# Optimization experiments

Hardware: AMD Instinct MI355X
Metric: run time of the kernel (lower is better)

The kernel has to match this reference:

```python
import jax, jax.numpy as jnp
import numpy as np

B, H, S, D = 4, 16, 2048, 64


def setup_inputs() -> dict:
    key = jax.random.key(0)
    kq, kk, kv, kp = jax.random.split(key, 4)
    query = jax.random.normal(kq, (B, H, S, D), dtype=jnp.float32)
    k = jax.random.normal(kk, (B, H, S, D), dtype=jnp.float32)
    value = jax.random.normal(kv, (B, H, S, D), dtype=jnp.float32)
    # 0/1 key-padding mask, broadcastable against the [S, S] causal mask
    padding_mask = jax.random.randint(kp, (B, 1, 1, S), 0, 2, dtype=jnp.int32)
    return {"query": query, "key": k, "value": value, "padding_mask": padding_mask}


def reference(query, key, value, padding_mask):
    d_k = query.shape[-1]
    seq_len = query.shape[-2]
    # scores: [B, H, S, S]
    scores = jnp.einsum("bhqd,bhkd->bhqk", query, key) / jnp.sqrt(jnp.float32(d_k))
    # causal mask: 1 above diagonal
    future = jnp.triu(jnp.ones((seq_len, seq_len), dtype=jnp.float32), k=1)
    combined = future + padding_mask.astype(jnp.float32)  # values in {0,1,2}
    # faithful to torch masked_fill(combined_mask == 1, -1e9): only exact 1 is masked
    scores = jnp.where(combined == 1.0, jnp.float32(-1e9), scores)
    attention_weights = jax.nn.softmax(scores, axis=-1)
    result = attention_weights @ value  # [B, H, S, D]
    return result, attention_weights
```

## Files before the change

### kernel.cpp

```cpp
#include <hip/hip_runtime.h>

#define SEQ 2048
#define DH  64
#define NH  16
#define NB  4
#define QT  64
#define NT  512
#define NHEADS (NB * NH)
#define NKT (SEQ / 64)
#define NBLK (NHEADS * (SEQ / QT))
#define TILE_ELEMS 4096

typedef _Float16 f16x8 __attribute__((ext_vector_type(8)));
typedef short    s16x8 __attribute__((ext_vector_type(8)));
typedef float    f32x4 __attribute__((ext_vector_type(4)));

static __device__ __forceinline__ int swe(int row, int col) {
    return (row << 6) + (col ^ ((row & 7) << 3));
}

static __device__ __forceinline__ void gload16(const void* g, void* l) {
    __builtin_amdgcn_global_load_lds(
        (const __attribute__((address_space(1))) void*)g,
        (__attribute__((address_space(3))) void*)l, 16, 0, 0);
}

static __device__ __forceinline__ short f16b(float x) {
    _Float16 h = (_Float16)x;
    return __builtin_bit_cast(short, h);
}

__global__ __launch_bounds__(256) void prep(
    const float* __restrict__ K, const float* __restrict__ V,
    const int* __restrict__ pad,
    short* __restrict__ kh, short* __restrict__ kl,
    short* __restrict__ vh, short* __restrict__ vl,
    unsigned* __restrict__ pm)
{
    const int t    = threadIdx.x;
    const int kt   = blockIdx.x & (NKT - 1);
    const int head = blockIdx.x >> 5;
    const size_t toff = ((size_t)head * NKT + kt) * TILE_ELEMS;
    const float* Kg = K + ((size_t)head * SEQ + (size_t)kt * 64) * DH;
    const float* Vg = V + ((size_t)head * SEQ + (size_t)kt * 64) * DH;

    {
        const int row = t >> 2;
        const int c0  = (t & 3) * 16;
        const float4* gp = (const float4*)(Kg + (size_t)row * DH + c0);
        const float4 v0 = gp[0], v1 = gp[1], v2 = gp[2], v3 = gp[3];
        const float x[16] = {v0.x,v0.y,v0.z,v0.w, v1.x,v1.y,v1.z,v1.w,
                             v2.x,v2.y,v2.z,v2.w, v3.x,v3.y,v3.z,v3.w};
        s16x8 hi[2], lo[2];
#pragma unroll
        for (int j = 0; j < 16; ++j) {
            _Float16 h = (_Float16)x[j];
            hi[j >> 3][j & 7] = __builtin_bit_cast(short, h);
            lo[j >> 3][j & 7] = f16b(x[j] - (float)h);
        }
        *(s16x8*)&kh[toff + swe(row, c0)]     = hi[0];
        *(s16x8*)&kh[toff + swe(row, c0 + 8)] = hi[1];
        *(s16x8*)&kl[toff + swe(row, c0)]     = lo[0];
        *(s16x8*)&kl[toff + swe(row, c0 + 8)] = lo[1];
    }
    {
#pragma unroll
        for (int half = 0; half < 2; ++half) {
            const int d  = t & 63;
            const int k0 = half * 32 + (t >> 6) * 8;
            s16x8 hi8, lo8;
#pragma unroll
            for (int i = 0; i < 8; ++i) {
                float x = Vg[(size_t)(k0 + i) * DH + d];
                _Float16 h = (_Float16)x;
                hi8[i] = __builtin_bit_cast(short, h);
                lo8[i] = f16b(x - (float)h);
            }
            *(s16x8*)&vh[toff + swe(d, k0)] = hi8;
            *(s16x8*)&vl[toff + swe(d, k0)] = lo8;
        }
    }
    if (blockIdx.x == 0) {
        const int b = t >> 6, klc = t & 63;
        unsigned mword = 0;
#pragma unroll
        for (int kt2 = 0; kt2 < NKT; ++kt2)
            mword |= (unsigned)(pad[b * SEQ + kt2 * 64 + klc] & 1) << kt2;
        pm[t] = mword;
    }
}

#define QK_TILE(kb_, A0, A1) do {                                                    \
  _Pragma("unroll") for (int dh = 0; dh < 2; ++dh) {                                 \
    const int d0_ = dh * 32 + lg * 8;                                                \
    const f16x8 bh = *(const f16x8*)&s_k[kb_][0][swe(key, d0_)];                     \
    const f16x8 bl = *(const f16x8*)&s_k[kb_][1][swe(key, d0_)];                     \
    A0 = __builtin_amdgcn_mfma_f32_16x16x32_f16(qfh[0][dh], bh, A0, 0, 0, 0);        \
    A1 = __builtin_amdgcn_mfma_f32_16x16x32_f16(qfh[1][dh], bh, A1, 0, 0, 0);        \
    A0 = __builtin_amdgcn_mfma_f32_16x16x32_f16(qfh[0][dh], bl, A0, 0, 0, 0);        \
    A1 = __builtin_amdgcn_mfma_f32_16x16x32_f16(qfh[1][dh], bl, A1, 0, 0, 0);        \
    A0 = __builtin_amdgcn_mfma_f32_16x16x32_f16(qfl[0][dh], bh, A0, 0, 0, 0);        \
    A1 = __builtin_amdgcn_mfma_f32_16x16x32_f16(qfl[1][dh], bh, A1, 0, 0, 0);        \
  } } while (0)

#define STAGE_K(buf_, kt_) do {                                                      \
    const size_t o_ = (size_t)(kt_) * TILE_ELEMS + (size_t)t * 8;                    \
    gload16(khh + o_, &s_k[buf_][0][w * 512]);                                       \
    gload16(klh + o_, &s_k[buf_][1][w * 512]);                                       \
} while (0)
#define STAGE_V(buf_, kt_) do {                                                      \
    const size_t o_ = (size_t)(kt_) * TILE_ELEMS + (size_t)t * 8;                    \
    gload16(vhh + o_, &s_vu.v[buf_][0][w * 512]);                                    \
    gload16(vlh + o_, &s_vu.v[buf_][1][w * 512]);                                    \
} while (0)

#define WAIT_BAR(cnt_) do {                                                          \
    asm volatile("s_waitcnt " cnt_ ::: "memory");                                    \
    __builtin_amdgcn_s_barrier();                                                    \
    __builtin_amdgcn_sched_barrier(0);                                               \
} while (0)

__global__ __launch_bounds__(NT, 4) void attn_fwd(
    const float* __restrict__ Q,
    const short* __restrict__ KH, const short* __restrict__ KL,
    const short* __restrict__ VH, const short* __restrict__ VL,
    const unsigned* __restrict__ PM,
    float* __restrict__ out_res, float* __restrict__ out_w)
{
    __shared__ __attribute__((aligned(16))) short s_k[2][2][TILE_ELEMS];
    __shared__ union __attribute__((aligned(16))) {
        short v[2][2][TILE_ELEMS];
        short q[2][TILE_ELEMS];
        float o[64][68];
    } s_vu;
    __shared__ __attribute__((aligned(16))) short s_w[TILE_ELEMS];
    __shared__ float s_red[64][4];

    const int t = threadIdx.x;
    int bid = blockIdx.x;
    bid = (bid & 7) * (NBLK / 8) + (bid >> 3);

    const int qtile = bid & (SEQ / QT - 1);
    const int head  = bid >> 5;
    const int q0    = qtile * QT;
    const size_t hoff = (size_t)head * SEQ * DH;
    const size_t woff = (size_t)head * SEQ * SEQ;

    const short* khh = KH + (size_t)head * NKT * TILE_ELEMS;
    const short* klh = KL + (size_t)head * NKT * TILE_ELEMS;
    const short* vhh = VH + (size_t)head * NKT * TILE_ELEMS;
    const short* vlh = VL + (size_t)head * NKT * TILE_ELEMS;

    const int l  = t & 63;
    const int w  = t >> 6;
    const int wq = w >> 2;
    const int wk = w & 3;
    const int lj = l & 15;
    const int lg = l >> 4;

    const int key = wk * 16 + lj;
    const unsigned pmask = PM[(head >> 4) * 64 + key];

    {
        const int row = t >> 3;
        const int c0  = (t & 7) * 8;
        const float* gp = Q + hoff + (size_t)(q0 + row) * DH + c0;
        const float4 a = *(const float4*)gp;
        const float4 b = *(const float4*)(gp + 4);
        const float x[8] = {a.x,a.y,a.z,a.w, b.x,b.y,b.z,b.w};
        s16x8 hi8, lo8;
#pragma unroll
        for (int j = 0; j < 8; ++j) {
            _Float16 h = (_Float16)x[j];
            hi8[j] = __builtin_bit_cast(short, h);
            lo8[j] = f16b(x[j] - (float)h);
        }
        *(s16x8*)&s_vu.q[0][swe(row, c0)] = hi8;
        *(s16x8*)&s_vu.q[1][swe(row, c0)] = lo8;
    }
    __syncthreads();

    f16x8 qfh[2][2], qfl[2][2];
#pragma unroll
    for (int m = 0; m < 2; ++m)
#pragma unroll
        for (int dh = 0; dh < 2; ++dh) {
            const int row = wq * 32 + m * 16 + lj;
            const int d0  = dh * 32 + lg * 8;
            qfh[m][dh] = *(const f16x8*)&s_vu.q[0][swe(row, d0)];
            qfl[m][dh] = *(const f16x8*)&s_vu.q[1][swe(row, d0)];
        }
    asm volatile("s_waitcnt lgkmcnt(0)" ::: "memory");
    __syncthreads();

    const int wk2   = wk >> 1;
    const int dbase = (wk & 1) * 32;
    const int ks    = wk2 * 32 + lg * 8;

    float rs[2][4] = {};
    f32x4 ov[2][2];
#pragma unroll
    for (int m = 0; m < 2; ++m)
#pragma unroll
        for (int n = 0; n < 2; ++n) ov[m][n] = (f32x4){0.f,0.f,0.f,0.f};

    STAGE_K(0, 0);
    STAGE_V(0, 0);
    WAIT_BAR("vmcnt(0)");

#pragma unroll 1
    for (int kt = 0; kt < NKT; ++kt) {
        const int cur = kt & 1, nxt = cur ^ 1;
        const int ktn = (kt + 1) & (NKT - 1);
        STAGE_K(nxt, ktn);
        STAGE_V(nxt, ktn);

        f32x4 a0 = {0.f,0.f,0.f,0.f}, a1 = {0.f,0.f,0.f,0.f};
        __builtin_amdgcn_s_setprio(1);
        QK_TILE(cur, a0, a1);
        __builtin_amdgcn_s_setprio(0);

        const int ka = kt * 64 + key;
        const int pd = (int)((pmask >> kt) & 1u);
#pragma unroll
        for (int m = 0; m < 2; ++m) {
            const f32x4 av = m ? a1 : a0;
            const int qrow = q0 + wq * 32 + m * 16 + lg * 4;
            const int qloc = wq * 32 + m * 16 + lg * 4;
#pragma unroll
            for (int r = 0; r < 4; ++r) {
                const bool msk = ((ka > qrow + r) != (pd == 1));
                const float s  = msk ? -8.0e9f : av[r];
                const float e  = __expf(s * 0.125f);
                rs[m][r] += e;
                s_w[swe(qloc + r, key)] = f16b(e);
            }
        }
        WAIT_BAR("lgkmcnt(0)");

        {
            const f16x8 aw0 = *(const f16x8*)&s_w[swe(wq * 32 + lj,      ks)];
            const f16x8 aw1 = *(const f16x8*)&s_w[swe(wq * 32 + 16 + lj, ks)];
            const f16x8 bh0 = *(const f16x8*)&s_vu.v[cur][0][swe(dbase + lj,      ks)];
            const f16x8 bh1 = *(const f16x8*)&s_vu.v[cur][0][swe(dbase + 16 + lj, ks)];
            const f16x8 bl0 = *(const f16x8*)&s_vu.v[cur][1][swe(dbase + lj,      ks)];
            const f16x8 bl1 = *(const f16x8*)&s_vu.v[cur][1][swe(dbase + 16 + lj, ks)];
            __builtin_amdgcn_s_setprio(1);
            ov[0][0] = __builtin_amdgcn_mfma_f32_16x16x32_f16(aw0, bh0, ov[0][0], 0,0,0);
            ov[0][1] = __builtin_amdgcn_mfma_f32_16x16x32_f16(aw0, bh1, ov[0][1], 0,0,0);
            ov[1][0] = __builtin_amdgcn_mfma_f32_16x16x32_f16(aw1, bh0, ov[1][0], 0,0,0);
            ov[1][1] = __builtin_amdgcn_mfma_f32_16x16x32_f16(aw1, bh1, ov[1][1], 0,0,0);
            ov[0][0] = __builtin_amdgcn_mfma_f32_16x16x32_f16(aw0, bl0, ov[0][0], 0,0,0);
            ov[0][1] = __builtin_amdgcn_mfma_f32_16x16x32_f16(aw0, bl1, ov[0][1], 0,0,0);
            ov[1][0] = __builtin_amdgcn_mfma_f32_16x16x32_f16(aw1, bl0, ov[1][0], 0,0,0);
            ov[1][1] = __builtin_amdgcn_mfma_f32_16x16x32_f16(aw1, bl1, ov[1][1], 0,0,0);
            __builtin_amdgcn_s_setprio(0);
        }
        WAIT_BAR("vmcnt(0)");
    }

#pragma unroll
    for (int m = 0; m < 2; ++m)
#pragma unroll
        for (int r = 0; r < 4; ++r) {
            float v = rs[m][r];
#pragma unroll
            for (int off = 1; off < 16; off <<= 1) v += __shfl_xor(v, off, 64);
            rs[m][r] = v;
        }
    if (lj == 0) {
#pragma unroll
        for (int m = 0; m < 2; ++m)
#pragma unroll
            for (int r = 0; r < 4; ++r)
                s_red[wq * 32 + m * 16 + lg * 4 + r][wk] = rs[m][r];
    }
    __syncthreads();
    float invr[2][4];
#pragma unroll
    for (int m = 0; m < 2; ++m)
#pragma unroll
        for (int r = 0; r < 4; ++r) {
            const int row = wq * 32 + m * 16 + lg * 4 + r;
            invr[m][r] = 1.0f / (s_red[row][0] + s_red[row][1] +
                                 s_red[row][2] + s_red[row][3]);
        }

#pragma unroll
    for (int m = 0; m < 2; ++m)
#pragma unroll
        for (int n = 0; n < 2; ++n)
#pragma unroll
            for (int r = 0; r < 4; ++r) ov[m][n][r] *= invr[m][r];

    if (wk2 == 0) {
#pragma unroll
        for (int m = 0; m < 2; ++m)
#pragma unroll
            for (int n = 0; n < 2; ++n)
#pragma unroll
                for (int r = 0; r < 4; ++r)
                    s_vu.o[wq * 32 + m * 16 + lg * 4 + r][dbase + n * 16 + lj] = ov[m][n][r];
    }
    __syncthreads();
    if (wk2 == 1) {
#pragma unroll
        for (int m = 0; m < 2; ++m)
#pragma unroll
            for (int n = 0; n < 2; ++n)
#pragma unroll
                for (int r = 0; r < 4; ++r)
                    s_vu.o[wq * 32 + m * 16 + lg * 4 + r][dbase + n * 16 + lj] += ov[m][n][r];
    }
    __syncthreads();
    {
        const int row = t >> 3;
        const int c0  = (t & 7) * 8;
        const float4 v0 = *(const float4*)&s_vu.o[row][c0];
        const float4 v1 = *(const float4*)&s_vu.o[row][c0 + 4];
        float* op = out_res + hoff + (size_t)(q0 + row) * DH + c0;
        *(float4*)op       = v0;
        *(float4*)(op + 4) = v1;
    }

#pragma unroll 1
    for (int kt = 0; kt < NKT; ++kt) {
        const int cur = kt & 1, nxt = cur ^ 1;
        STAGE_K(nxt, (kt + 1) & (NKT - 1));

        f32x4 a0 = {0.f,0.f,0.f,0.f}, a1 = {0.f,0.f,0.f,0.f};
        __builtin_amdgcn_s_setprio(1);
        QK_TILE(cur, a0, a1);
        __builtin_amdgcn_s_setprio(0);

        const int ka = kt * 64 + key;
        const int pd = (int)((pmask >> kt) & 1u);
#pragma unroll
        for (int m = 0; m < 2; ++m) {
            const f32x4 av = m ? a1 : a0;
            const int qrow = q0 + wq * 32 + m * 16 + lg * 4;
#pragma unroll
            for (int r = 0; r < 4; ++r) {
                const bool msk = ((ka > qrow + r) != (pd == 1));
                const float s  = msk ? -8.0e9f : av[r];
                const float e  = __expf(s * 0.125f);
                out_w[woff + (size_t)(qrow + r) * SEQ + ka] = e * invr[m][r];
            }
        }
        WAIT_BAR("vmcnt(8)");
    }
}

extern "C" void kernel_launch(void* const* d_in, const int* in_sizes, int n_in,
                              void* d_out, int out_size, void* d_ws, size_t ws_size,
                              hipStream_t stream) {
    const float* Q   = (const float*)d_in[0];
    const float* K   = (const float*)d_in[1];
    const float* V   = (const float*)d_in[2];
    const int*   pad = (const int*)d_in[3];
    float* out_res = (float*)d_out;
    float* out_w   = out_res + (size_t)NB * NH * SEQ * DH;

    const size_t T = (size_t)NHEADS * NKT * TILE_ELEMS;
    short* kh = (short*)d_ws;
    short* kl = kh + T;
    short* vh = kl + T;
    short* vl = vh + T;
    unsigned* pm = (unsigned*)(vl + T);

    prep<<<dim3(NHEADS * NKT), 256, 0, stream>>>(K, V, pad, kh, kl, vh, vl, pm);
    attn_fwd<<<dim3(NBLK), NT, 0, stream>>>(Q, kh, kl, vh, vl, pm, out_res, out_w);
}
```

Baseline: 1.466 ms.

## Software-pipeline PV matmul one tile behind QK and use nontemporal weight stores

The first pass now double-buffers the softmax weight tile and runs the P·V MFMAs for the previous key tile after computing QK for the current one, so each iteration needs one barrier instead of two. V loads are issued per tile just after the barrier, and the first K load is moved ahead of the Q conversion. The second pass moves its barrier to the top of the loop, and the attention-weight writes become nontemporal stores to avoid polluting cache. Shared memory is reorganised: s_red now aliases the weight buffer and the output staging aliases the V buffers. V now has less lead time before it is consumed, which could expose load latency.

New measurement: 1.376 ms. 1.06x faster.

```diff
diff --git a/kernel.cpp b/kernel.cpp
--- a/kernel.cpp
+++ b/kernel.cpp
@@ -103,6 +103,25 @@
     A1 = __builtin_amdgcn_mfma_f32_16x16x32_f16(qfl[1][dh], bh, A1, 0, 0, 0);        \
   } } while (0)
 
+#define PV_TILE(prv_) do {                                                           \
+    const f16x8 aw0 = *(const f16x8*)&s_wq.w[prv_][swe(wq * 32 + lj,      ks)];      \
+    const f16x8 aw1 = *(const f16x8*)&s_wq.w[prv_][swe(wq * 32 + 16 + lj, ks)];      \
+    const f16x8 bh0 = *(const f16x8*)&s_vo.v[prv_][0][swe(dbase + lj,      ks)];     \
+    const f16x8 bh1 = *(const f16x8*)&s_vo.v[prv_][0][swe(dbase + 16 + lj, ks)];     \
+    const f16x8 bl0 = *(const f16x8*)&s_vo.v[prv_][1][swe(dbase + lj,      ks)];     \
+    const f16x8 bl1 = *(const f16x8*)&s_vo.v[prv_][1][swe(dbase + 16 + lj, ks)];     \
+    __builtin_amdgcn_s_setprio(1);                                                   \
+    ov[0][0] = __builtin_amdgcn_mfma_f32_16x16x32_f16(aw0, bh0, ov[0][0], 0,0,0);    \
+    ov[0][1] = __builtin_amdgcn_mfma_f32_16x16x32_f16(aw0, bh1, ov[0][1], 0,0,0);    \
+    ov[1][0] = __builtin_amdgcn_mfma_f32_16x16x32_f16(aw1, bh0, ov[1][0], 0,0,0);    \
+    ov[1][1] = __builtin_amdgcn_mfma_f32_16x16x32_f16(aw1, bh1, ov[1][1], 0,0,0);    \
+    ov[0][0] = __builtin_amdgcn_mfma_f32_16x16x32_f16(aw0, bl0, ov[0][0], 0,0,0);    \
+    ov[0][1] = __builtin_amdgcn_mfma_f32_16x16x32_f16(aw0, bl1, ov[0][1], 0,0,0);    \
+    ov[1][0] = __builtin_amdgcn_mfma_f32_16x16x32_f16(aw1, bl0, ov[1][0], 0,0,0);    \
+    ov[1][1] = __builtin_amdgcn_mfma_f32_16x16x32_f16(aw1, bl1, ov[1][1], 0,0,0);    \
+    __builtin_amdgcn_s_setprio(0);                                                   \
+} while (0)
+
 #define STAGE_K(buf_, kt_) do {                                                      \
     const size_t o_ = (size_t)(kt_) * TILE_ELEMS + (size_t)t * 8;                    \
     gload16(khh + o_, &s_k[buf_][0][w * 512]);                                       \
@@ -110,11 +129,11 @@
 } while (0)
 #define STAGE_V(buf_, kt_) do {                                                      \
     const size_t o_ = (size_t)(kt_) * TILE_ELEMS + (size_t)t * 8;                    \
-    gload16(vhh + o_, &s_vu.v[buf_][0][w * 512]);                                    \
-    gload16(vlh + o_, &s_vu.v[buf_][1][w * 512]);                                    \
+    gload16(vhh + o_, &s_vo.v[buf_][0][w * 512]);                                    \
+    gload16(vlh + o_, &s_vo.v[buf_][1][w * 512]);                                    \
 } while (0)
 
-#define WAIT_BAR(cnt_) do {                                                          \
+#define PIPE_BAR(cnt_) do {                                                          \
     asm volatile("s_waitcnt " cnt_ ::: "memory");                                    \
     __builtin_amdgcn_s_barrier();                                                    \
     __builtin_amdgcn_sched_barrier(0);                                               \
@@ -130,11 +149,13 @@
     __shared__ __attribute__((aligned(16))) short s_k[2][2][TILE_ELEMS];
     __shared__ union __attribute__((aligned(16))) {
         short v[2][2][TILE_ELEMS];
+        float o[64][68];
+    } s_vo;
+    __shared__ union __attribute__((aligned(16))) {
+        short w[2][TILE_ELEMS];
         short q[2][TILE_ELEMS];
-        float o[64][68];
-    } s_vu;
-    __shared__ __attribute__((aligned(16))) short s_w[TILE_ELEMS];
-    __shared__ float s_red[64][4];
+    } s_wq;
+    float (*s_red)[4] = reinterpret_cast<float (*)[4]>(&s_wq.w[0][0]);
 
     const int t = threadIdx.x;
     int bid = blockIdx.x;
@@ -160,6 +181,12 @@
 
     const int key = wk * 16 + lj;
     const unsigned pmask = PM[(head >> 4) * 64 + key];
+
+    const int wk2   = wk >> 1;
+    const int dbase = (wk & 1) * 32;
+    const int ks    = wk2 * 32 + lg * 8;
+
+    STAGE_K(0, 0);
 
     {
         const int row = t >> 3;
@@ -175,8 +202,8 @@
             hi8[j] = __builtin_bit_cast(short, h);
             lo8[j] = f16b(x[j] - (float)h);
         }
-        *(s16x8*)&s_vu.q[0][swe(row, c0)] = hi8;
-        *(s16x8*)&s_vu.q[1][swe(row, c0)] = lo8;
+        *(s16x8*)&s_wq.q[0][swe(row, c0)] = hi8;
+        *(s16x8*)&s_wq.q[1][swe(row, c0)] = lo8;
     }
     __syncthreads();
 
@@ -187,15 +214,11 @@
         for (int dh = 0; dh < 2; ++dh) {
             const int row = wq * 32 + m * 16 + lj;
             const int d0  = dh * 32 + lg * 8;
-            qfh[m][dh] = *(const f16x8*)&s_vu.q[0][swe(row, d0)];
-            qfl[m][dh] = *(const f16x8*)&s_vu.q[1][swe(row, d0)];
+            qfh[m][dh] = *(const f16x8*)&s_wq.q[0][swe(row, d0)];
+            qfl[m][dh] = *(const f16x8*)&s_wq.q[1][swe(row, d0)];
         }
     asm volatile("s_waitcnt lgkmcnt(0)" ::: "memory");
     __syncthreads();
-
-    const int wk2   = wk >> 1;
-    const int dbase = (wk & 1) * 32;
-    const int ks    = wk2 * 32 + lg * 8;
 
     float rs[2][4] = {};
     f32x4 ov[2][2];
@@ -204,16 +227,12 @@
 #pragma unroll
         for (int n = 0; n < 2; ++n) ov[m][n] = (f32x4){0.f,0.f,0.f,0.f};
 
-    STAGE_K(0, 0);
-    STAGE_V(0, 0);
-    WAIT_BAR("vmcnt(0)");
-
 #pragma unroll 1
     for (int kt = 0; kt < NKT; ++kt) {
-        const int cur = kt & 1, nxt = cur ^ 1;
-        const int ktn = (kt + 1) & (NKT - 1);
-        STAGE_K(nxt, ktn);
-        STAGE_V(nxt, ktn);
+        const int cur = kt & 1, prv = cur ^ 1;
+        PIPE_BAR("vmcnt(0) lgkmcnt(0)");
+        STAGE_V(cur, kt);
+        STAGE_K(prv, (kt + 1) & (NKT - 1));
 
         f32x4 a0 = {0.f,0.f,0.f,0.f}, a1 = {0.f,0.f,0.f,0.f};
         __builtin_amdgcn_s_setprio(1);
@@ -233,31 +252,14 @@
                 const float s  = msk ? -8.0e9f : av[r];
                 const float e  = __expf(s * 0.125f);
                 rs[m][r] += e;
-                s_w[swe(qloc + r, key)] = f16b(e);
+                s_wq.w[cur][swe(qloc + r, key)] = f16b(e);
             }
         }
-        WAIT_BAR("lgkmcnt(0)");
-
-        {
-            const f16x8 aw0 = *(const f16x8*)&s_w[swe(wq * 32 + lj,      ks)];
-            const f16x8 aw1 = *(const f16x8*)&s_w[swe(wq * 32 + 16 + lj, ks)];
-            const f16x8 bh0 = *(const f16x8*)&s_vu.v[cur][0][swe(dbase + lj,      ks)];
-            const f16x8 bh1 = *(const f16x8*)&s_vu.v[cur][0][swe(dbase + 16 + lj, ks)];
-            const f16x8 bl0 = *(const f16x8*)&s_vu.v[cur][1][swe(dbase + lj,      ks)];
-            const f16x8 bl1 = *(const f16x8*)&s_vu.v[cur][1][swe(dbase + 16 + lj, ks)];
-            __builtin_amdgcn_s_setprio(1);
-            ov[0][0] = __builtin_amdgcn_mfma_f32_16x16x32_f16(aw0, bh0, ov[0][0], 0,0,0);
-            ov[0][1] = __builtin_amdgcn_mfma_f32_16x16x32_f16(aw0, bh1, ov[0][1], 0,0,0);
-            ov[1][0] = __builtin_amdgcn_mfma_f32_16x16x32_f16(aw1, bh0, ov[1][0], 0,0,0);
-            ov[1][1] = __builtin_amdgcn_mfma_f32_16x16x32_f16(aw1, bh1, ov[1][1], 0,0,0);
-            ov[0][0] = __builtin_amdgcn_mfma_f32_16x16x32_f16(aw0, bl0, ov[0][0], 0,0,0);
-            ov[0][1] = __builtin_amdgcn_mfma_f32_16x16x32_f16(aw0, bl1, ov[0][1], 0,0,0);
-            ov[1][0] = __builtin_amdgcn_mfma_f32_16x16x32_f16(aw1, bl0, ov[1][0], 0,0,0);
-            ov[1][1] = __builtin_amdgcn_mfma_f32_16x16x32_f16(aw1, bl1, ov[1][1], 0,0,0);
-            __builtin_amdgcn_s_setprio(0);
-        }
-        WAIT_BAR("vmcnt(0)");
-    }
+
+        if (kt > 0) PV_TILE(prv);
+    }
+    PIPE_BAR("vmcnt(0) lgkmcnt(0)");
+    PV_TILE(1);
 
 #pragma unroll
     for (int m = 0; m < 2; ++m)
@@ -300,7 +302,7 @@
             for (int n = 0; n < 2; ++n)
 #pragma unroll
                 for (int r = 0; r < 4; ++r)
-                    s_vu.o[wq * 32 + m * 16 + lg * 4 + r][dbase + n * 16 + lj] = ov[m][n][r];
+                    s_vo.o[wq * 32 + m * 16 + lg * 4 + r][dbase + n * 16 + lj] = ov[m][n][r];
     }
     __syncthreads();
     if (wk2 == 1) {
@@ -310,14 +312,14 @@
             for (int n = 0; n < 2; ++n)
 #pragma unroll
                 for (int r = 0; r < 4; ++r)
-                    s_vu.o[wq * 32 + m * 16 + lg * 4 + r][dbase + n * 16 + lj] += ov[m][n][r];
+                    s_vo.o[wq * 32 + m * 16 + lg * 4 + r][dbase + n * 16 + lj] += ov[m][n][r];
     }
     __syncthreads();
     {
         const int row = t >> 3;
         const int c0  = (t & 7) * 8;
-        const float4 v0 = *(const float4*)&s_vu.o[row][c0];
-        const float4 v1 = *(const float4*)&s_vu.o[row][c0 + 4];
+        const float4 v0 = *(const float4*)&s_vo.o[row][c0];
+        const float4 v1 = *(const float4*)&s_vo.o[row][c0 + 4];
         float* op = out_res + hoff + (size_t)(q0 + row) * DH + c0;
         *(float4*)op       = v0;
         *(float4*)(op + 4) = v1;
@@ -326,6 +328,7 @@
 #pragma unroll 1
     for (int kt = 0; kt < NKT; ++kt) {
         const int cur = kt & 1, nxt = cur ^ 1;
+        PIPE_BAR("vmcnt(8)");
         STAGE_K(nxt, (kt + 1) & (NKT - 1));
 
         f32x4 a0 = {0.f,0.f,0.f,0.f}, a1 = {0.f,0.f,0.f,0.f};
@@ -344,10 +347,10 @@
                 const bool msk = ((ka > qrow + r) != (pd == 1));
                 const float s  = msk ? -8.0e9f : av[r];
                 const float e  = __expf(s * 0.125f);
-                out_w[woff + (size_t)(qrow + r) * SEQ + ka] = e * invr[m][r];
+                __builtin_nontemporal_store(e * invr[m][r],
+                    &out_w[woff + (size_t)(qrow + r) * SEQ + ka]);
             }
         }
-        WAIT_BAR("vmcnt(8)");
     }
 }
 
```
